# Optimization experiments

Hardware: AMD Instinct MI355X
Metric: run time of the kernel (lower is better)

Reference implementation:

```python
import jax, jax.numpy as jnp
import numpy as np

NUM_PATCHES = 128  # static stand-in for max(patch_ids)+1


def setup_inputs() -> dict:
    key = jax.random.key(0)
    k1, k2, k3, k4 = jax.random.split(key, 4)
    B, S, H, D = 8, 8192, 512, 768
    byte_hiddens = jax.random.normal(k1, (B, S, H), dtype=jnp.float32)
    patch_ids = jnp.sort(jax.random.randint(k2, (B, S), 0, NUM_PATCHES), axis=-1)
    # Dense output_projection (glorot-uniform-ish init)
    lim = float(np.sqrt(6.0 / (H + D)))
    W_proj = jax.random.uniform(k3, (H, D), minval=-lim, maxval=lim, dtype=jnp.float32)
    b_proj = jnp.zeros((D,), dtype=jnp.float32)
    return {"byte_hiddens": byte_hiddens, "W_proj": W_proj, "b_proj": b_proj,
            "patch_ids": patch_ids}


def reference(byte_hiddens, W_proj, b_proj, patch_ids):
    # Mean pooling within patches: for each patch p, mean of byte_hiddens where
    # patch_ids == p (sum / max(count, 1)), then Dense projection.
    B, S, H = byte_hiddens.shape
    P = NUM_PATCHES
    # Flatten batch into segment ids so one segment_sum covers all (b, p) pairs.
    seg = (patch_ids + jnp.arange(B, dtype=patch_ids.dtype)[:, None] * P).reshape(-1)
    flat = byte_hiddens.reshape(B * S, H)
    sums = jax.ops.segment_sum(flat, seg, num_segments=B * P)          # [B*P, H]
    counts = jax.ops.segment_sum(jnp.ones((B * S,), byte_hiddens.dtype), seg,
                                 num_segments=B * P)                   # [B*P]
    means = sums / jnp.maximum(counts, 1.0)[:, None]                   # [B*P, H]
    means = means.reshape(B, P, H)
    return means @ W_proj + b_proj                                     # [B, P, D]
```

## Files before the change

kernel.cpp:

```cpp
#include <hip/hip_runtime.h>

#define B_ 8
#define S_ 8192
#define H_ 512
#define D_ 768
#define P_ 128

typedef __attribute__((ext_vector_type(8))) short bf16x8;
typedef __attribute__((ext_vector_type(4))) float f32x4;

static __device__ inline unsigned short f2bf(float f) {
    unsigned int u = __float_as_uint(f);
    unsigned int r = (u + 0x7fffu + ((u >> 16) & 1u)) >> 16;
    return (unsigned short)r;
}


__global__ __launch_bounds__(256) void wt_kernel(
    const float* __restrict__ W, unsigned short* __restrict__ Wt)
{
    const int nb = blockIdx.x * 64;
    const int kb = blockIdx.y * 64;
    __shared__ unsigned short T[64][72];
    const int t = threadIdx.x;
    {
        const int kk = t >> 4;
        const int nn = (t & 15) * 4;
        #pragma unroll
        for (int i = 0; i < 4; ++i) {
            float4 v = *(const float4*)&W[(size_t)(kb + kk + i * 16) * D_ + nb + nn];
            T[nn + 0][kk + i * 16] = f2bf(v.x);
            T[nn + 1][kk + i * 16] = f2bf(v.y);
            T[nn + 2][kk + i * 16] = f2bf(v.z);
            T[nn + 3][kk + i * 16] = f2bf(v.w);
        }
    }
    __syncthreads();
    {
        const int nn = t >> 4;
        const int kk = (t & 15) * 4;
        #pragma unroll
        for (int i = 0; i < 4; ++i) {
            ushort4 o;
            o.x = T[nn + i * 16][kk + 0];
            o.y = T[nn + i * 16][kk + 1];
            o.z = T[nn + i * 16][kk + 2];
            o.w = T[nn + i * 16][kk + 3];
            *(ushort4*)&Wt[(size_t)(nb + nn + i * 16) * H_ + kb + kk] = o;
        }
    }
}

__global__ __launch_bounds__(256) void pool_kernel(
    const float* __restrict__ bh, const int* __restrict__ ids,
    unsigned short* __restrict__ means)
{
    const int p = blockIdx.x;
    const int b = blockIdx.y;
    const int t = threadIdx.x;
    const int c = t & 127;
    const int r_ofs = t >> 7;

    const int* row = ids + (size_t)b * S_;
    int lo0 = 0, hi0 = S_, lo1 = 0, hi1 = S_;
    #pragma unroll
    for (int it = 0; it < 13; ++it) {
        int m0 = (lo0 + hi0) >> 1, m1 = (lo1 + hi1) >> 1;
        int v0 = row[m0], v1 = row[m1];
        if (v0 < p)  lo0 = m0 + 1; else hi0 = m0;
        if (v1 <= p) lo1 = m1 + 1; else hi1 = m1;
    }
    const int start = lo0;
    const int cnt   = lo1 - lo0;

    const float4* src = (const float4*)(bh + ((size_t)b * S_ + (size_t)start) * H_) + c;
    float4 a0 = {0.f, 0.f, 0.f, 0.f};
    float4 a1 = {0.f, 0.f, 0.f, 0.f};
    int r = r_ofs;
    for (; r + 2 < cnt; r += 4) {
        float4 v0 = src[(size_t)r * (H_ / 4)];
        float4 v1 = src[(size_t)(r + 2) * (H_ / 4)];
        a0.x += v0.x; a0.y += v0.y; a0.z += v0.z; a0.w += v0.w;
        a1.x += v1.x; a1.y += v1.y; a1.z += v1.z; a1.w += v1.w;
    }
    if (r < cnt) {
        float4 v = src[(size_t)r * (H_ / 4)];
        a0.x += v.x; a0.y += v.y; a0.z += v.z; a0.w += v.w;
    }
    float4 s;
    s.x = a0.x + a1.x; s.y = a0.y + a1.y; s.z = a0.z + a1.z; s.w = a0.w + a1.w;

    __shared__ float4 red[128];
    if (r_ofs == 1) red[c] = s;
    __syncthreads();
    if (r_ofs == 0) {
        float4 o = red[c];
        const float inv = 1.0f / (float)(cnt > 0 ? cnt : 1);
        ushort4 w;
        w.x = f2bf((s.x + o.x) * inv);
        w.y = f2bf((s.y + o.y) * inv);
        w.z = f2bf((s.z + o.z) * inv);
        w.w = f2bf((s.w + o.w) * inv);
        *(ushort4*)&means[((size_t)(b * P_ + p)) * H_ + c * 4] = w;
    }
}

__global__ __launch_bounds__(256) void gemm_kernel(
    const unsigned short* __restrict__ A, const unsigned short* __restrict__ Bt,
    const float* __restrict__ bias, float* __restrict__ C)
{
    __shared__ unsigned short As[64][40];
    __shared__ unsigned short Bs[64][40];

    const int t    = threadIdx.x;
    const int lane = t & 63;
    const int wv   = t >> 6;
    const int mrow = lane & 15;
    const int quad = lane >> 4;
    const int m0   = blockIdx.y * 64;
    const int n0   = blockIdx.x * 64;

    const int sr = t >> 2;
    const int sk = (t & 3) * 8;
    const unsigned short* Aptr = A  + (size_t)(m0 + sr) * H_ + sk;
    const unsigned short* Bptr = Bt + (size_t)(n0 + sr) * H_ + sk;

    uint4 a_reg = *(const uint4*)Aptr;
    uint4 b_reg = *(const uint4*)Bptr;

    f32x4 acc[4] = {};

    for (int k0 = 0; k0 < H_; k0 += 32) {
        *(uint4*)&As[sr][sk] = a_reg;
        *(uint4*)&Bs[sr][sk] = b_reg;
        __syncthreads();

        if (k0 + 32 < H_) {
            a_reg = *(const uint4*)(Aptr + k0 + 32);
            b_reg = *(const uint4*)(Bptr + k0 + 32);
        }

        #pragma unroll
        for (int kk = 0; kk < 2; ++kk) {
        }
        {
            bf16x8 af = *(const bf16x8*)&As[wv * 16 + mrow][quad * 8];
            #pragma unroll
            for (int t4 = 0; t4 < 4; ++t4) {
                bf16x8 bf = *(const bf16x8*)&Bs[t4 * 16 + mrow][quad * 8];
                acc[t4] = __builtin_amdgcn_mfma_f32_16x16x32_bf16(af, bf, acc[t4], 0, 0, 0);
            }
        }
        __syncthreads();
    }

    #pragma unroll
    for (int t4 = 0; t4 < 4; ++t4) {
        const int col = n0 + t4 * 16 + mrow;
        const float bia = bias[col];
        #pragma unroll
        for (int r = 0; r < 4; ++r) {
            const int rowi = m0 + wv * 16 + quad * 4 + r;
            C[(size_t)rowi * D_ + col] = acc[t4][r] + bia;
        }
    }
}

extern "C" void kernel_launch(void* const* d_in, const int* in_sizes, int n_in,
                              void* d_out, int out_size, void* d_ws, size_t ws_size,
                              hipStream_t stream) {
    const float* bh   = (const float*)d_in[0];
    const float* W    = (const float*)d_in[1];
    const float* bias = (const float*)d_in[2];
    const int*   ids  = (const int*)d_in[3];
    float* out = (float*)d_out;

    unsigned short* means = (unsigned short*)d_ws;
    unsigned short* Wt    = means + (size_t)B_ * P_ * H_;

    wt_kernel<<<dim3(D_ / 64, H_ / 64), 256, 0, stream>>>(W, Wt);
    pool_kernel<<<dim3(P_, B_), 256, 0, stream>>>(bh, ids, means);
    gemm_kernel<<<dim3(D_ / 64, (B_ * P_) / 64), 256, 0, stream>>>(
        means, Wt, bias, out);
}
```

Baseline: 210.2 us.

## Merge pooling and weight transpose into one launch; use 64-wide K tiles in GEMM

The weight transpose/convert kernel and the pooling kernel are combined into a single launch that dispatches on block index, removing one kernel launch and letting the small transpose work overlap with the bandwidth-bound pooling. The GEMM's K tile doubles from 32 to 64, so each iteration issues two MFMA steps per barrier pair and the number of synchronisations is halved. The trade-off is larger shared-memory tiles and more registers for the staged loads.

```diff
diff --git a/kernel.cpp b/kernel.cpp
--- a/kernel.cpp
+++ b/kernel.cpp
@@ -16,92 +16,94 @@
 }
 
 
-__global__ __launch_bounds__(256) void wt_kernel(
-    const float* __restrict__ W, unsigned short* __restrict__ Wt)
+__global__ __launch_bounds__(256) void pool_wt_kernel(
+    const float* __restrict__ bh, const int* __restrict__ ids,
+    const float* __restrict__ W,
+    unsigned short* __restrict__ means, unsigned short* __restrict__ Wt)
 {
-    const int nb = blockIdx.x * 64;
-    const int kb = blockIdx.y * 64;
-    __shared__ unsigned short T[64][72];
+    __shared__ __align__(16) char smem[64 * 72 * sizeof(unsigned short)];
+    const int bid = blockIdx.x;
     const int t = threadIdx.x;
-    {
-        const int kk = t >> 4;
-        const int nn = (t & 15) * 4;
+
+    if (bid < P_ * B_) {
+        const int p = bid & (P_ - 1);
+        const int b = bid >> 7;
+        const int c = t & 127;
+        const int r_ofs = t >> 7;
+
+        const int* row = ids + (size_t)b * S_;
+        int lo0 = 0, hi0 = S_, lo1 = 0, hi1 = S_;
         #pragma unroll
-        for (int i = 0; i < 4; ++i) {
-            float4 v = *(const float4*)&W[(size_t)(kb + kk + i * 16) * D_ + nb + nn];
-            T[nn + 0][kk + i * 16] = f2bf(v.x);
-            T[nn + 1][kk + i * 16] = f2bf(v.y);
-            T[nn + 2][kk + i * 16] = f2bf(v.z);
-            T[nn + 3][kk + i * 16] = f2bf(v.w);
+        for (int it = 0; it < 13; ++it) {
+            int m0 = (lo0 + hi0) >> 1, m1 = (lo1 + hi1) >> 1;
+            int v0 = row[m0], v1 = row[m1];
+            if (v0 < p)  lo0 = m0 + 1; else hi0 = m0;
+            if (v1 <= p) lo1 = m1 + 1; else hi1 = m1;
         }
-    }
-    __syncthreads();
-    {
-        const int nn = t >> 4;
-        const int kk = (t & 15) * 4;
-        #pragma unroll
-        for (int i = 0; i < 4; ++i) {
-            ushort4 o;
-            o.x = T[nn + i * 16][kk + 0];
-            o.y = T[nn + i * 16][kk + 1];
-            o.z = T[nn + i * 16][kk + 2];
-            o.w = T[nn + i * 16][kk + 3];
-            *(ushort4*)&Wt[(size_t)(nb + nn + i * 16) * H_ + kb + kk] = o;
+        const int start = lo0;
+        const int cnt   = lo1 - lo0;
+
+        const float4* src = (const float4*)(bh + ((size_t)b * S_ + (size_t)start) * H_) + c;
+        float4 a0 = {0.f, 0.f, 0.f, 0.f};
+        float4 a1 = {0.f, 0.f, 0.f, 0.f};
+        int r = r_ofs;
+        for (; r + 2 < cnt; r += 4) {
+            float4 v0 = src[(size_t)r * (H_ / 4)];
+            float4 v1 = src[(size_t)(r + 2) * (H_ / 4)];
+            a0.x += v0.x; a0.y += v0.y; a0.z += v0.z; a0.w += v0.w;
+            a1.x += v1.x; a1.y += v1.y; a1.z += v1.z; a1.w += v1.w;
         }
-    }
-}
+        if (r < cnt) {
+            float4 v = src[(size_t)r * (H_ / 4)];
+            a0.x += v.x; a0.y += v.y; a0.z += v.z; a0.w += v.w;
+        }
+        float4 s;
+        s.x = a0.x + a1.x; s.y = a0.y + a1.y; s.z = a0.z + a1.z; s.w = a0.w + a1.w;
 
-__global__ __launch_bounds__(256) void pool_kernel(
-    const float* __restrict__ bh, const int* __restrict__ ids,
-    unsigned short* __restrict__ means)
-{
-    const int p = blockIdx.x;
-    const int b = blockIdx.y;
-    const int t = threadIdx.x;
-    const int c = t & 127;
-    const int r_ofs = t >> 7;
-
-    const int* row = ids + (size_t)b * S_;
-    int lo0 = 0, hi0 = S_, lo1 = 0, hi1 = S_;
-    #pragma unroll
-    for (int it = 0; it < 13; ++it) {
-        int m0 = (lo0 + hi0) >> 1, m1 = (lo1 + hi1) >> 1;
-        int v0 = row[m0], v1 = row[m1];
-        if (v0 < p)  lo0 = m0 + 1; else hi0 = m0;
-        if (v1 <= p) lo1 = m1 + 1; else hi1 = m1;
-    }
-    const int start = lo0;
-    const int cnt   = lo1 - lo0;
-
-    const float4* src = (const float4*)(bh + ((size_t)b * S_ + (size_t)start) * H_) + c;
-    float4 a0 = {0.f, 0.f, 0.f, 0.f};
-    float4 a1 = {0.f, 0.f, 0.f, 0.f};
-    int r = r_ofs;
-    for (; r + 2 < cnt; r += 4) {
-        float4 v0 = src[(size_t)r * (H_ / 4)];
-        float4 v1 = src[(size_t)(r + 2) * (H_ / 4)];
-        a0.x += v0.x; a0.y += v0.y; a0.z += v0.z; a0.w += v0.w;
-        a1.x += v1.x; a1.y += v1.y; a1.z += v1.z; a1.w += v1.w;
-    }
-    if (r < cnt) {
-        float4 v = src[(size_t)r * (H_ / 4)];
-        a0.x += v.x; a0.y += v.y; a0.z += v.z; a0.w += v.w;
-    }
-    float4 s;
-    s.x = a0.x + a1.x; s.y = a0.y + a1.y; s.z = a0.z + a1.z; s.w = a0.w + a1.w;
-
-    __shared__ float4 red[128];
-    if (r_ofs == 1) red[c] = s;
-    __syncthreads();
-    if (r_ofs == 0) {
-        float4 o = red[c];
-        const float inv = 1.0f / (float)(cnt > 0 ? cnt : 1);
-        ushort4 w;
-        w.x = f2bf((s.x + o.x) * inv);
-        w.y = f2bf((s.y + o.y) * inv);
-        w.z = f2bf((s.z + o.z) * inv);
-        w.w = f2bf((s.w + o.w) * inv);
-        *(ushort4*)&means[((size_t)(b * P_ + p)) * H_ + c * 4] = w;
+        float4* red = (float4*)smem;
+        if (r_ofs == 1) red[c] = s;
+        __syncthreads();
+        if (r_ofs == 0) {
+            float4 o = red[c];
+            const float inv = 1.0f / (float)(cnt > 0 ? cnt : 1);
+            ushort4 w;
+            w.x = f2bf((s.x + o.x) * inv);
+            w.y = f2bf((s.y + o.y) * inv);
+            w.z = f2bf((s.z + o.z) * inv);
+            w.w = f2bf((s.w + o.w) * inv);
+            *(ushort4*)&means[((size_t)(b * P_ + p)) * H_ + c * 4] = w;
+        }
+    } else {
+        const int id = bid - P_ * B_;
+        const int nb = (id % (D_ / 64)) * 64;
+        const int kb = (id / (D_ / 64)) * 64;
+        unsigned short (*T)[72] = (unsigned short (*)[72])smem;
+        {
+            const int kk = t >> 4;
+            const int nn = (t & 15) * 4;
+            #pragma unroll
+            for (int i = 0; i < 4; ++i) {
+                float4 v = *(const float4*)&W[(size_t)(kb + kk + i * 16) * D_ + nb + nn];
+                T[nn + 0][kk + i * 16] = f2bf(v.x);
+                T[nn + 1][kk + i * 16] = f2bf(v.y);
+                T[nn + 2][kk + i * 16] = f2bf(v.z);
+                T[nn + 3][kk + i * 16] = f2bf(v.w);
+            }
+        }
+        __syncthreads();
+        {
+            const int nn = t >> 4;
+            const int kk = (t & 15) * 4;
+            #pragma unroll
+            for (int i = 0; i < 4; ++i) {
+                ushort4 o;
+                o.x = T[nn + i * 16][kk + 0];
+                o.y = T[nn + i * 16][kk + 1];
+                o.z = T[nn + i * 16][kk + 2];
+                o.w = T[nn + i * 16][kk + 3];
+                *(ushort4*)&Wt[(size_t)(nb + nn + i * 16) * H_ + kb + kk] = o;
+            }
+        }
     }
 }
 
@@ -109,8 +111,8 @@
     const unsigned short* __restrict__ A, const unsigned short* __restrict__ Bt,
     const float* __restrict__ bias, float* __restrict__ C)
 {
-    __shared__ unsigned short As[64][40];
-    __shared__ unsigned short Bs[64][40];
+    __shared__ unsigned short As[64][72];
+    __shared__ unsigned short Bs[64][72];
 
     const int t    = threadIdx.x;
     const int lane = t & 63;
@@ -121,33 +123,37 @@
     const int n0   = blockIdx.x * 64;
 
     const int sr = t >> 2;
-    const int sk = (t & 3) * 8;
+    const int sk = (t & 3) * 16;
     const unsigned short* Aptr = A  + (size_t)(m0 + sr) * H_ + sk;
     const unsigned short* Bptr = Bt + (size_t)(n0 + sr) * H_ + sk;
 
-    uint4 a_reg = *(const uint4*)Aptr;
-    uint4 b_reg = *(const uint4*)Bptr;
+    uint4 a0 = *(const uint4*)Aptr;
+    uint4 a1 = *(const uint4*)(Aptr + 8);
+    uint4 b0 = *(const uint4*)Bptr;
+    uint4 b1 = *(const uint4*)(Bptr + 8);
 
     f32x4 acc[4] = {};
 
-    for (int k0 = 0; k0 < H_; k0 += 32) {
-        *(uint4*)&As[sr][sk] = a_reg;
-        *(uint4*)&Bs[sr][sk] = b_reg;
+    for (int k0 = 0; k0 < H_; k0 += 64) {
+        *(uint4*)&As[sr][sk]     = a0;
+        *(uint4*)&As[sr][sk + 8] = a1;
+        *(uint4*)&Bs[sr][sk]     = b0;
+        *(uint4*)&Bs[sr][sk + 8] = b1;
         __syncthreads();
 
-        if (k0 + 32 < H_) {
-            a_reg = *(const uint4*)(Aptr + k0 + 32);
-            b_reg = *(const uint4*)(Bptr + k0 + 32);
+        if (k0 + 64 < H_) {
+            a0 = *(const uint4*)(Aptr + k0 + 64);
+            a1 = *(const uint4*)(Aptr + k0 + 72);
+            b0 = *(const uint4*)(Bptr + k0 + 64);
+            b1 = *(const uint4*)(Bptr + k0 + 72);
         }
 
         #pragma unroll
         for (int kk = 0; kk < 2; ++kk) {
-        }
-        {
-            bf16x8 af = *(const bf16x8*)&As[wv * 16 + mrow][quad * 8];
+            bf16x8 af = *(const bf16x8*)&As[wv * 16 + mrow][kk * 32 + quad * 8];
             #pragma unroll
             for (int t4 = 0; t4 < 4; ++t4) {
-                bf16x8 bf = *(const bf16x8*)&Bs[t4 * 16 + mrow][quad * 8];
+                bf16x8 bf = *(const bf16x8*)&Bs[t4 * 16 + mrow][kk * 32 + quad * 8];
                 acc[t4] = __builtin_amdgcn_mfma_f32_16x16x32_bf16(af, bf, acc[t4], 0, 0, 0);
             }
         }
@@ -178,8 +184,8 @@
     unsigned short* means = (unsigned short*)d_ws;
     unsigned short* Wt    = means + (size_t)B_ * P_ * H_;
 
-    wt_kernel<<<dim3(D_ / 64, H_ / 64), 256, 0, stream>>>(W, Wt);
-    pool_kernel<<<dim3(P_, B_), 256, 0, stream>>>(bh, ids, means);
+    pool_wt_kernel<<<dim3(P_ * B_ + (D_ / 64) * (H_ / 64)), 256, 0, stream>>>(
+        bh, ids, W, means, Wt);
     gemm_kernel<<<dim3(D_ / 64, (B_ * P_) / 64), 256, 0, stream>>>(
         means, Wt, bias, out);
 }
```

Result: no change. 207.4 us (-1.3%).
